# Kernel tuning notes

Measured on AMD Instinct MI355X. Metric: run time of the kernel, lower is better.

Reference implementation:

```python
import jax, jax.numpy as jnp
import numpy as np


def setup_inputs() -> dict:
    key = jax.random.key(0)
    k1, k2 = jax.random.split(key)
    x = jax.random.normal(k1, (16384, 1024), dtype=jnp.float32)
    prototypes = jax.random.normal(k2, (2048, 1024), dtype=jnp.float32)
    alpha = jnp.ones((1,), dtype=jnp.float32)
    return {"x": x, "prototypes": prototypes, "alpha": alpha}


def reference(x, prototypes, alpha):
    # distance_matrix[n,k] = (alpha + 1e-16)^2 * ||x_n - p_k||^2
    x_sq = jnp.sum(x * x, axis=-1, keepdims=True)              # [N,1]
    p_sq = jnp.sum(prototypes * prototypes, axis=-1)[None, :]  # [1,K]
    cross = jnp.einsum('nd,kd->nk', x, prototypes)             # [N,K]
    sq_dist = x_sq + p_sq - 2.0 * cross                        # [N,K]
    scale = jnp.square(alpha + 1e-16)                          # [1]
    return scale * sq_dist
```

## Files before the change

kernel.cpp:

```cpp
#include <hip/hip_runtime.h>
#include <hip/hip_fp16.h>


#define N_ROWS 16384
#define K_PROTO 2048
#define DIM 1024

#define BM 256
#define BN 256
#define BK 64
#define NT (DIM / BK)
#define NHT (4 * NT)

typedef _Float16 half8 __attribute__((ext_vector_type(8)));
typedef float f32x4 __attribute__((ext_vector_type(4)));

__device__ __forceinline__ void async_copy16(void* lds_dst, const void* g_src) {
    __builtin_amdgcn_global_load_lds(
        (const __attribute__((address_space(1))) void*)g_src,
        (__attribute__((address_space(3))) void*)lds_dst,
        16, 0, 0);
}

__global__ __launch_bounds__(256) void convert_kernel(
    const float* __restrict__ x, const float* __restrict__ p,
    __half* __restrict__ xh, __half* __restrict__ ph,
    float* __restrict__ xsq, float* __restrict__ psq)
{
    int row = blockIdx.x;
    const float* src;
    __half* dst;
    float* sq;
    if (row < N_ROWS) {
        src = x + (size_t)row * DIM;
        dst = xh + (size_t)row * DIM;
        sq = xsq + row;
    } else {
        int r = row - N_ROWS;
        src = p + (size_t)r * DIM;
        dst = ph + (size_t)r * DIM;
        sq = psq + r;
    }
    int t = threadIdx.x;
    float4 v = reinterpret_cast<const float4*>(src)[t];
    float s = v.x * v.x + v.y * v.y + v.z * v.z + v.w * v.w;

    union { __half2 h[2]; uint2 u; } pk;
    pk.h[0] = __floats2half2_rn(v.x, v.y);
    pk.h[1] = __floats2half2_rn(v.z, v.w);
    reinterpret_cast<uint2*>(dst)[t] = pk.u;

    #pragma unroll
    for (int off = 32; off > 0; off >>= 1) s += __shfl_down(s, off);
    __shared__ float red[4];
    if ((t & 63) == 0) red[t >> 6] = s;
    __syncthreads();
    if (t == 0) sq[0] = red[0] + red[1] + red[2] + red[3];
}


#define LDA(mo)                                                                      \
    do {                                                                             \
        _Pragma("unroll")                                                            \
        for (int m_ = 0; m_ < 4; ++m_) {                                             \
            const int row_ = wm * 128 + ((mo) + m_) * 16 + rr;                       \
            _Pragma("unroll")                                                        \
            for (int kk_ = 0; kk_ < 2; ++kk_)                                        \
                Af[m_][kk_] = *(const half8*)(Ab + row_ * 128 +                      \
                                   (((kk_ * 4 + lq) ^ (row_ & 7)) << 4));            \
        }                                                                            \
    } while (0)

#define LDB(n)                                                                       \
    do {                                                                             \
        const int row_ = wn * 64 + (n) * 16 + rr;                                    \
        _Pragma("unroll")                                                            \
        for (int kk_ = 0; kk_ < 2; ++kk_)                                            \
            Bf[n][kk_] = *(const half8*)(Bb + row_ * 128 +                           \
                               (((kk_ * 4 + lq) ^ (row_ & 7)) << 4));                \
    } while (0)

#define MMA8(mo, n0)                                                                 \
    do {                                                                             \
        _Pragma("unroll")                                                            \
        for (int m_ = 0; m_ < 4; ++m_)                                               \
            _Pragma("unroll")                                                        \
            for (int n_ = 0; n_ < 2; ++n_)                                           \
                _Pragma("unroll")                                                    \
                for (int kk_ = 0; kk_ < 2; ++kk_)                                    \
                    acc[(mo) + m_][(n0) + n_] =                                      \
                        __builtin_amdgcn_mfma_f32_16x16x32_f16(                      \
                            Af[m_][kk_], Bf[(n0) + n_][kk_],                         \
                            acc[(mo) + m_][(n0) + n_], 0, 0, 0);                     \
    } while (0)

#define PHASE_MID()                                                                  \
    __builtin_amdgcn_s_barrier();                                                    \
    asm volatile("s_waitcnt lgkmcnt(0)" ::: "memory");                               \
    __builtin_amdgcn_s_setprio(1)

#define PHASE_END()                                                                  \
    __builtin_amdgcn_s_setprio(0);                                                   \
    __builtin_amdgcn_s_barrier()

__global__ __launch_bounds__(512, 2) void gemm8_kernel(
    const __half* __restrict__ xh, const __half* __restrict__ ph,
    const float* __restrict__ xsq, const float* __restrict__ psq,
    const float* __restrict__ alpha, float* __restrict__ out)
{
    extern __shared__ char lds[];

    const int tid = threadIdx.x;
    const int w = tid >> 6, lane = tid & 63;
    const int wm = w >> 2, wn = w & 3;
    const int rr = lane & 15, lq = lane >> 4;

    const int bid = blockIdx.x;
    const int swz = (bid & 7) * 64 + (bid >> 3);
    const int bm = swz >> 3, bn = swz & 7;

    const __half* Abase = xh + (size_t)bm * BM * DIM;
    const __half* Bbase = ph + (size_t)bn * BN * DIM;

    f32x4 acc[8][4];
    #pragma unroll
    for (int m = 0; m < 8; ++m)
        #pragma unroll
        for (int n = 0; n < 4; ++n)
            acc[m][n] = (f32x4)0.0f;

    auto stage_ht = [&](int s) {
        if (s >= NHT) return;
        const int T = s >> 2, j = s & 3;
        char* buf = lds + (size_t)(T & 1) * 65536;
        const bool isA = (j >= 2);
        const int rowoff = (j & 1) << 7;
        const __half* gb = isA ? Abase : Bbase;
        char* region = buf + (isA ? 0 : 32768) + rowoff * 128;
        #pragma unroll
        for (int i = 0; i < 2; ++i) {
            const int c = i * 512 + tid;
            const int r = c >> 3;
            const int sl = (c & 7) ^ (r & 7);
            async_copy16(region + c * 16,
                         gb + (size_t)(rowoff + r) * DIM + T * BK + sl * 8);
        }
    };

    half8 Af[4][2], Bf[4][2];
    const char *Ab, *Bb;

    #pragma unroll
    for (int s = 0; s < 7; ++s) stage_ht(s);
    asm volatile("s_waitcnt vmcnt(6)" ::: "memory");
    __builtin_amdgcn_s_barrier();

    for (int t = 0; t < NT; ++t) {
        const char* base = lds + (size_t)(t & 1) * 65536;
        Ab = base; Bb = base + 32768;
        const int p = t * 4;

        LDA(0); LDB(0); LDB(1);
        stage_ht(p + 7);
        asm volatile("s_waitcnt lgkmcnt(4)" ::: "memory");
        PHASE_MID();
        MMA8(0, 0);
        PHASE_END();

        LDB(2); LDB(3);
        stage_ht(p + 8);
        PHASE_MID();
        MMA8(0, 2);
        PHASE_END();

        LDA(4);
        stage_ht(p + 9);
        asm volatile("s_waitcnt lgkmcnt(4)" ::: "memory");
        PHASE_MID();
        MMA8(4, 2);
        PHASE_END();

        stage_ht(p + 10);
        __builtin_amdgcn_s_barrier();
        asm volatile("s_waitcnt lgkmcnt(0)" ::: "memory");
        __builtin_amdgcn_s_setprio(1);
        MMA8(4, 0);
        __builtin_amdgcn_s_setprio(0);
        if (t == NT - 2)
            asm volatile("s_waitcnt vmcnt(0)" ::: "memory");
        else if (t < NT - 2)
            asm volatile("s_waitcnt vmcnt(6)" ::: "memory");
        __builtin_amdgcn_s_barrier();
    }

    const float a = alpha[0] + 1e-16f;
    const float scale = a * a;
    const int row0 = bm * BM + wm * 128 + lq * 4;
    const int col0 = bn * BN + wn * 64 + rr;
    #pragma unroll
    for (int n = 0; n < 4; ++n) {
        const int col = col0 + n * 16;
        const float pv = psq[col];
        #pragma unroll
        for (int m = 0; m < 8; ++m) {
            const int rbase = row0 + m * 16;
            #pragma unroll
            for (int r = 0; r < 4; ++r) {
                const int row = rbase + r;
                out[(size_t)row * K_PROTO + col] =
                    scale * (xsq[row] + pv - 2.0f * acc[m][n][r]);
            }
        }
    }
}

__global__ __launch_bounds__(256) void fallback_kernel(
    const float* __restrict__ x, const float* __restrict__ p,
    const float* __restrict__ alpha, float* __restrict__ out)
{
    __shared__ float xs[DIM];
    int n = blockIdx.x;
    int t = threadIdx.x;
    reinterpret_cast<float4*>(xs)[t] = reinterpret_cast<const float4*>(x + (size_t)n * DIM)[t];
    __syncthreads();
    const float a = alpha[0] + 1e-16f;
    const float scale = a * a;
    for (int j = 0; j < K_PROTO / 256; ++j) {
        int k = j * 256 + t;
        const float4* pr = reinterpret_cast<const float4*>(p + (size_t)k * DIM);
        float s = 0.0f;
        #pragma unroll 8
        for (int d4 = 0; d4 < DIM / 4; ++d4) {
            float4 pv = pr[d4];
            float dx = xs[d4 * 4 + 0] - pv.x;
            float dy = xs[d4 * 4 + 1] - pv.y;
            float dz = xs[d4 * 4 + 2] - pv.z;
            float dw = xs[d4 * 4 + 3] - pv.w;
            s += dx * dx + dy * dy + dz * dz + dw * dw;
        }
        out[(size_t)n * K_PROTO + k] = scale * s;
    }
}

extern "C" void kernel_launch(void* const* d_in, const int* in_sizes, int n_in,
                              void* d_out, int out_size, void* d_ws, size_t ws_size,
                              hipStream_t stream) {
    const float* x = (const float*)d_in[0];
    const float* p = (const float*)d_in[1];
    const float* alpha = (const float*)d_in[2];
    float* out = (float*)d_out;

    const size_t XH_BYTES = (size_t)N_ROWS * DIM * sizeof(__half);
    const size_t PH_BYTES = (size_t)K_PROTO * DIM * sizeof(__half);
    const size_t NEED = XH_BYTES + PH_BYTES +
                        (size_t)(N_ROWS + K_PROTO) * sizeof(float);

    if (ws_size < NEED) {
        fallback_kernel<<<dim3(N_ROWS), dim3(256), 0, stream>>>(x, p, alpha, out);
        return;
    }

    char* w = (char*)d_ws;
    __half* xh = (__half*)w;
    __half* ph = (__half*)(w + XH_BYTES);
    float* xsq = (float*)(w + XH_BYTES + PH_BYTES);
    float* psq = (float*)(w + XH_BYTES + PH_BYTES + N_ROWS * sizeof(float));

    convert_kernel<<<dim3(N_ROWS + K_PROTO), dim3(256), 0, stream>>>(
        x, p, xh, ph, xsq, psq);
    gemm8_kernel<<<dim3((N_ROWS / BM) * (K_PROTO / BN)), dim3(512), 131072, stream>>>(
        xh, ph, xsq, psq, alpha, out);
}
```

Baseline: 281.4 us.

## Reorder GEMM phase schedule with double A-fragment registers and vectorized xsq loads

Restructures the per-K-tile loop so all B fragments load up front and the second half of the A fragments goes into a separate register set (Afh), prefetched during the first MMA phases. The staging order of the A and B half-tiles is changed so the data each phase needs arrives earlier, and LDS waits are relaxed to let more loads stay in flight while MFMAs run. The epilogue now loads xsq as float4 once per row group instead of a scalar load per element. The extra fragment registers raise register pressure on a kernel targeting 2 blocks per CU at 512 threads.

```diff
diff --git a/kernel.cpp b/kernel.cpp
--- a/kernel.cpp
+++ b/kernel.cpp
@@ -59,14 +59,14 @@
 }
 
 
-#define LDA(mo)                                                                      \
+#define LDA_(dst, mo)                                                                \
     do {                                                                             \
         _Pragma("unroll")                                                            \
         for (int m_ = 0; m_ < 4; ++m_) {                                             \
             const int row_ = wm * 128 + ((mo) + m_) * 16 + rr;                       \
             _Pragma("unroll")                                                        \
             for (int kk_ = 0; kk_ < 2; ++kk_)                                        \
-                Af[m_][kk_] = *(const half8*)(Ab + row_ * 128 +                      \
+                dst[m_][kk_] = *(const half8*)(Ab + row_ * 128 +                     \
                                    (((kk_ * 4 + lq) ^ (row_ & 7)) << 4));            \
         }                                                                            \
     } while (0)
@@ -80,7 +80,7 @@
                                (((kk_ * 4 + lq) ^ (row_ & 7)) << 4));                \
     } while (0)
 
-#define MMA8(mo, n0)                                                                 \
+#define MMA8_(A_, mo, n0)                                                            \
     do {                                                                             \
         _Pragma("unroll")                                                            \
         for (int m_ = 0; m_ < 4; ++m_)                                               \
@@ -90,18 +90,9 @@
                 for (int kk_ = 0; kk_ < 2; ++kk_)                                    \
                     acc[(mo) + m_][(n0) + n_] =                                      \
                         __builtin_amdgcn_mfma_f32_16x16x32_f16(                      \
-                            Af[m_][kk_], Bf[(n0) + n_][kk_],                         \
+                            A_[m_][kk_], Bf[(n0) + n_][kk_],                         \
                             acc[(mo) + m_][(n0) + n_], 0, 0, 0);                     \
     } while (0)
-
-#define PHASE_MID()                                                                  \
-    __builtin_amdgcn_s_barrier();                                                    \
-    asm volatile("s_waitcnt lgkmcnt(0)" ::: "memory");                               \
-    __builtin_amdgcn_s_setprio(1)
-
-#define PHASE_END()                                                                  \
-    __builtin_amdgcn_s_setprio(0);                                                   \
-    __builtin_amdgcn_s_barrier()
 
 __global__ __launch_bounds__(512, 2) void gemm8_kernel(
     const __half* __restrict__ xh, const __half* __restrict__ ph,
@@ -133,8 +124,8 @@
         if (s >= NHT) return;
         const int T = s >> 2, j = s & 3;
         char* buf = lds + (size_t)(T & 1) * 65536;
-        const bool isA = (j >= 2);
-        const int rowoff = (j & 1) << 7;
+        const bool isA = (j == 0) | (j == 3);
+        const int rowoff = ((j == 2) | (j == 3)) ? 128 : 0;
         const __half* gb = isA ? Abase : Bbase;
         char* region = buf + (isA ? 0 : 32768) + rowoff * 128;
         #pragma unroll
@@ -147,7 +138,7 @@
         }
     };
 
-    half8 Af[4][2], Bf[4][2];
+    half8 Af[4][2], Afh[4][2], Bf[4][2];
     const char *Ab, *Bb;
 
     #pragma unroll
@@ -158,33 +149,38 @@
     for (int t = 0; t < NT; ++t) {
         const char* base = lds + (size_t)(t & 1) * 65536;
         Ab = base; Bb = base + 32768;
-        const int p = t * 4;
-
-        LDA(0); LDB(0); LDB(1);
-        stage_ht(p + 7);
+        const int p4 = t * 4;
+
+        LDA_(Af, 0); LDB(0); LDB(1); LDB(2); LDB(3);
+        stage_ht(p4 + 7);
+        __builtin_amdgcn_s_barrier();
         asm volatile("s_waitcnt lgkmcnt(4)" ::: "memory");
-        PHASE_MID();
-        MMA8(0, 0);
-        PHASE_END();
-
-        LDB(2); LDB(3);
-        stage_ht(p + 8);
-        PHASE_MID();
-        MMA8(0, 2);
-        PHASE_END();
-
-        LDA(4);
-        stage_ht(p + 9);
-        asm volatile("s_waitcnt lgkmcnt(4)" ::: "memory");
-        PHASE_MID();
-        MMA8(4, 2);
-        PHASE_END();
-
-        stage_ht(p + 10);
+        __builtin_amdgcn_s_setprio(1);
+        MMA8_(Af, 0, 0);
+        __builtin_amdgcn_s_setprio(0);
+        __builtin_amdgcn_s_barrier();
+
+        LDA_(Afh, 4);
+        stage_ht(p4 + 8);
+        __builtin_amdgcn_s_barrier();
+        asm volatile("s_waitcnt lgkmcnt(8)" ::: "memory");
+        __builtin_amdgcn_s_setprio(1);
+        MMA8_(Af, 0, 2);
+        __builtin_amdgcn_s_setprio(0);
+        __builtin_amdgcn_s_barrier();
+
+        stage_ht(p4 + 9);
         __builtin_amdgcn_s_barrier();
         asm volatile("s_waitcnt lgkmcnt(0)" ::: "memory");
         __builtin_amdgcn_s_setprio(1);
-        MMA8(4, 0);
+        MMA8_(Afh, 4, 2);
+        __builtin_amdgcn_s_setprio(0);
+        __builtin_amdgcn_s_barrier();
+
+        stage_ht(p4 + 10);
+        __builtin_amdgcn_s_barrier();
+        __builtin_amdgcn_s_setprio(1);
+        MMA8_(Afh, 4, 0);
         __builtin_amdgcn_s_setprio(0);
         if (t == NT - 2)
             asm volatile("s_waitcnt vmcnt(0)" ::: "memory");
@@ -197,6 +193,10 @@
     const float scale = a * a;
     const int row0 = bm * BM + wm * 128 + lq * 4;
     const int col0 = bn * BN + wn * 64 + rr;
+    float4 xs4[8];
+    #pragma unroll
+    for (int m = 0; m < 8; ++m)
+        xs4[m] = *reinterpret_cast<const float4*>(xsq + row0 + m * 16);
     #pragma unroll
     for (int n = 0; n < 4; ++n) {
         const int col = col0 + n * 16;
@@ -206,9 +206,10 @@
             const int rbase = row0 + m * 16;
             #pragma unroll
             for (int r = 0; r < 4; ++r) {
-                const int row = rbase + r;
-                out[(size_t)row * K_PROTO + col] =
-                    scale * (xsq[row] + pv - 2.0f * acc[m][n][r]);
+                const float xv = (r == 0) ? xs4[m].x : (r == 1) ? xs4[m].y
+                               : (r == 2) ? xs4[m].z : xs4[m].w;
+                out[(size_t)(rbase + r) * K_PROTO + col] =
+                    scale * (xv + pv - 2.0f * acc[m][n][r]);
             }
         }
     }
```

Result: no change. 278.8 us (-0.9%).
